# Performance work log

Measured on AMD Instinct MI355X. Metric: run time of the kernel, lower is better.

The kernel has to match this reference:

```python
import jax, jax.numpy as jnp
import numpy as np

N_NODES = 100000
N_EDGES = 1600000
N_QEDGES = 400000
NUM_FEAT = 128
HIDDEN_C = 128
OUT_C = 64
NO_HEADS = 8


def setup_inputs() -> dict:
    key = jax.random.key(0)
    ks = jax.random.split(key, 8)
    x = jax.random.normal(ks[0], (N_NODES, NUM_FEAT), dtype=jnp.float32)
    W1 = jax.random.normal(ks[1], (NUM_FEAT, HIDDEN_C), dtype=jnp.float32) * (1.0 / np.sqrt(NUM_FEAT))
    b1 = jnp.zeros((HIDDEN_C,), dtype=jnp.float32)
    W2 = jax.random.normal(ks[2], (HIDDEN_C, OUT_C * NO_HEADS), dtype=jnp.float32) * (1.0 / np.sqrt(HIDDEN_C))
    b2 = jnp.zeros((OUT_C * NO_HEADS,), dtype=jnp.float32)
    edge_index = jax.random.randint(ks[3], (2, N_EDGES), 0, N_NODES, dtype=jnp.int32)
    q_edge_index = jax.random.randint(ks[4], (2, N_QEDGES), 0, N_NODES, dtype=jnp.int32)
    y = jax.random.randint(ks[5], (N_NODES,), 0, NO_HEADS, dtype=jnp.int32)
    return {"x": x, "W1": W1, "b1": b1, "W2": W2, "b2": b2,
            "edge_index": edge_index, "q_edge_index": q_edge_index, "y": y}


def gcn_conv(x, W, b, src, dst, n):
    """GCNConv: symmetric normalization with implicit self-loops."""
    h = x @ W  # [n, out]
    ones = jnp.ones(src.shape[0], dtype=x.dtype)
    deg = jax.ops.segment_sum(ones, dst, num_segments=n) + 1.0  # self-loop
    dinv = jax.lax.rsqrt(deg)
    norm = dinv[src] * dinv[dst]  # [E]
    agg = jax.ops.segment_sum(h[src] * norm[:, None], dst, num_segments=n)
    agg = agg + h * (dinv * dinv)[:, None]  # self-loop message
    return agg + b


def reference(x, W1, b1, W2, b2, edge_index, q_edge_index, y):
    src, dst = edge_index[0], edge_index[1]
    n = x.shape[0]
    hiddens = jax.nn.relu(gcn_conv(x, W1, b1, src, dst, n))            # [N, H]
    emb = gcn_conv(hiddens, W2, b2, src, dst, n)                        # [N, heads*out]
    emb = emb.reshape(n, NO_HEADS, OUT_C)                               # [N, h, f]
    q_row, q_col = q_edge_index[0], q_edge_index[1]
    preds = jnp.einsum('ehf,ehf->eh', emb[q_row], emb[q_col])           # [Q, h]
    pred_i = jnp.take_along_axis(preds, y[q_row][:, None].astype(jnp.int32), axis=1)[:, 0]
    pred_j = jnp.take_along_axis(preds, y[q_col][:, None].astype(jnp.int32), axis=1)[:, 0]
    pred = (pred_i + pred_j) * 0.5  # multiheads=True branch
    return hiddens, emb, pred_i, pred_j, pred
```

## Files before the change

kernel.cpp:

```cpp
#include <hip/hip_runtime.h>
#include <hip/hip_bf16.h>


#define SCAN_SEG 512

typedef short bf16x8 __attribute__((ext_vector_type(8)));
typedef float f32x4  __attribute__((ext_vector_type(4)));

__device__ __forceinline__ ushort f2bf(float x) {
    return (ushort)(__float_as_uint(x) >> 16);
}
__device__ __forceinline__ float bf2f(ushort h) {
    return __uint_as_float(((unsigned)h) << 16);
}

__global__ void count_kernel(const int* __restrict__ dst, int* __restrict__ cnt, int E) {
    int e = blockIdx.x * blockDim.x + threadIdx.x;
    if (e < E) atomicAdd(&cnt[dst[e]], 1);
}

__global__ __launch_bounds__(256) void blocksum_kernel(const int* __restrict__ cnt,
                                                       int* __restrict__ blocksum, int n) {
    __shared__ int red[4];
    int b = blockIdx.x, t = threadIdx.x;
    int i0 = b * SCAN_SEG + t;
    int s = 0;
    if (i0 < n) s += cnt[i0];
    if (i0 + 256 < n) s += cnt[i0 + 256];
#pragma unroll
    for (int off = 32; off >= 1; off >>= 1) s += __shfl_xor(s, off, 64);
    if ((t & 63) == 0) red[t >> 6] = s;
    __syncthreads();
    if (t == 0) blocksum[b] = red[0] + red[1] + red[2] + red[3];
}

__global__ __launch_bounds__(256) void blockscan_kernel(const int* __restrict__ blocksum,
                                                        int* __restrict__ blockoff, int nb,
                                                        int* __restrict__ row_ptr, int n, int E) {
    __shared__ int s[256];
    int t = threadIdx.x;
    int v = (t < nb) ? blocksum[t] : 0;
    s[t] = v;
    __syncthreads();
    for (int off = 1; off < 256; off <<= 1) {
        int u = (t >= off) ? s[t - off] : 0;
        __syncthreads();
        s[t] += u;
        __syncthreads();
    }
    if (t < nb) blockoff[t] = s[t] - v;
    if (t == 0) row_ptr[n] = E;
}

__global__ __launch_bounds__(256) void csr_ptr_kernel(const int* __restrict__ cnt,
                                                      const int* __restrict__ blockoff,
                                                      int* __restrict__ row_ptr,
                                                      int* __restrict__ cursor,
                                                      float* __restrict__ dinv, int n) {
    __shared__ int s[256];
    int b = blockIdx.x, t = threadIdx.x;
    int i0 = b * SCAN_SEG + 2 * t;
    int c0 = (i0     < n) ? cnt[i0]     : 0;
    int c1 = (i0 + 1 < n) ? cnt[i0 + 1] : 0;
    int pair = c0 + c1;
    s[t] = pair;
    __syncthreads();
    for (int off = 1; off < 256; off <<= 1) {
        int u = (t >= off) ? s[t - off] : 0;
        __syncthreads();
        s[t] += u;
        __syncthreads();
    }
    int excl = s[t] - pair + blockoff[b];
    if (i0 < n) {
        row_ptr[i0] = excl;
        cursor[i0]  = excl;
        dinv[i0]    = rsqrtf((float)(c0 + 1));
    }
    if (i0 + 1 < n) {
        row_ptr[i0 + 1] = excl + c0;
        cursor[i0 + 1]  = excl + c0;
        dinv[i0 + 1]    = rsqrtf((float)(c1 + 1));
    }
}

__global__ void fill_kernel(const int* __restrict__ src, const int* __restrict__ dst,
                            int* __restrict__ cursor, const float* __restrict__ dinv,
                            int* __restrict__ csr_src, float* __restrict__ csr_wt, int E) {
    int e = blockIdx.x * blockDim.x + threadIdx.x;
    if (e < E) {
        int s = src[e], d = dst[e];
        int pos = atomicAdd(&cursor[d], 1);
        csr_src[pos] = s;
        csr_wt[pos]  = dinv[s] * dinv[d];
    }
}

__global__ __launch_bounds__(128) void agg_kernel(const float* __restrict__ feat,
                                                  const int* __restrict__ row_ptr,
                                                  const int* __restrict__ csr_src,
                                                  const float* __restrict__ csr_wt,
                                                  const float* __restrict__ dinv,
                                                  float* __restrict__ out, int n) {
    int node = blockIdx.x;
    int f = threadIdx.x;
    float di = dinv[node];
    float acc = feat[(size_t)node * 128 + f] * di * di;
    int e0 = row_ptr[node], e1 = row_ptr[node + 1];
    int e = e0;
    for (; e + 4 <= e1; e += 4) {
        int s0 = csr_src[e],   s1 = csr_src[e+1], s2 = csr_src[e+2], s3 = csr_src[e+3];
        float w0 = csr_wt[e],  w1 = csr_wt[e+1],  w2 = csr_wt[e+2],  w3 = csr_wt[e+3];
        float v0 = feat[(size_t)s0 * 128 + f];
        float v1 = feat[(size_t)s1 * 128 + f];
        float v2 = feat[(size_t)s2 * 128 + f];
        float v3 = feat[(size_t)s3 * 128 + f];
        acc += v0 * w0 + v1 * w1 + v2 * w2 + v3 * w3;
    }
    for (; e < e1; ++e)
        acc += feat[(size_t)csr_src[e] * 128 + f] * csr_wt[e];
    out[(size_t)node * 128 + f] = acc;
}

__global__ __launch_bounds__(256, 2) void gemm_mfma(const float* __restrict__ X,
                                                    const float* __restrict__ W,
                                                    const float* __restrict__ bias,
                                                    float* __restrict__ C,
                                                    int N, int ldw, int do_relu) {
    __shared__ ushort Xh[128 * 64];
    __shared__ ushort Xl[128 * 64];
    __shared__ ushort Wh[128 * 64];
    __shared__ ushort Wl[128 * 64];

    const int tid  = threadIdx.x;
    const int lane = tid & 63;
    const int wv   = tid >> 6;
    const int wr   = wv >> 1;
    const int wc   = wv & 1;
    const int lr   = lane & 15;
    const int lk   = lane >> 4;
    const int row0   = blockIdx.y * 128;
    const int colOff = blockIdx.x * 128;

    f32x4 acc[4][4];
#pragma unroll
    for (int i = 0; i < 4; ++i)
#pragma unroll
        for (int j = 0; j < 4; ++j)
            acc[i][j] = (f32x4){0.f, 0.f, 0.f, 0.f};

    for (int ph = 0; ph < 2; ++ph) {
        if (ph) __syncthreads();

        {
#pragma unroll
            for (int j = 0; j < 8; ++j) {
                int e   = tid + 256 * j;
                int row = e >> 4;
                int k4  = e & 15;
                int gr  = row0 + row; if (gr >= N) gr = N - 1;
                float4 v = *(const float4*)(X + (size_t)gr * 128 + ph * 64 + k4 * 4);
                ushort4 h, l;
                h.x = f2bf(v.x); h.y = f2bf(v.y); h.z = f2bf(v.z); h.w = f2bf(v.w);
                l.x = f2bf(v.x - bf2f(h.x));
                l.y = f2bf(v.y - bf2f(h.y));
                l.z = f2bf(v.z - bf2f(h.z));
                l.w = f2bf(v.w - bf2f(h.w));
                int byte = row * 128 + ((k4 * 8) ^ ((row & 7) << 4));
                *(ushort4*)((char*)Xh + byte) = h;
                *(ushort4*)((char*)Xl + byte) = l;
            }
        }
        {
            const int c4 = tid & 31;
            const int kg = tid >> 5;
#pragma unroll
            for (int q = 0; q < 2; ++q) {
                int kloc  = kg * 8 + q * 4;
                int kglob = ph * 64 + kloc;
                const float* wp = W + (size_t)kglob * ldw + colOff + c4 * 4;
                float4 v0 = *(const float4*)(wp);
                float4 v1 = *(const float4*)(wp + ldw);
                float4 v2 = *(const float4*)(wp + 2 * (size_t)ldw);
                float4 v3 = *(const float4*)(wp + 3 * (size_t)ldw);
#pragma unroll
                for (int j = 0; j < 4; ++j) {
                    float a0 = (&v0.x)[j], a1 = (&v1.x)[j], a2 = (&v2.x)[j], a3 = (&v3.x)[j];
                    ushort4 h, l;
                    h.x = f2bf(a0); h.y = f2bf(a1); h.z = f2bf(a2); h.w = f2bf(a3);
                    l.x = f2bf(a0 - bf2f(h.x));
                    l.y = f2bf(a1 - bf2f(h.y));
                    l.z = f2bf(a2 - bf2f(h.z));
                    l.w = f2bf(a3 - bf2f(h.w));
                    int col  = c4 * 4 + j;
                    int byte = col * 128 + ((kloc * 2) ^ ((col & 7) << 4));
                    *(ushort4*)((char*)Wh + byte) = h;
                    *(ushort4*)((char*)Wl + byte) = l;
                }
            }
        }
        __syncthreads();

#pragma unroll
        for (int kk = 0; kk < 2; ++kk) {
            const int kb2 = (kk * 32 + lk * 8) * 2;
            bf16x8 ah[4], al[4], bh[4], bl[4];
#pragma unroll
            for (int mi = 0; mi < 4; ++mi) {
                int row  = wr * 64 + mi * 16 + lr;
                int byte = row * 128 + (kb2 ^ ((row & 7) << 4));
                ah[mi] = *(const bf16x8*)((const char*)Xh + byte);
                al[mi] = *(const bf16x8*)((const char*)Xl + byte);
            }
#pragma unroll
            for (int ni = 0; ni < 4; ++ni) {
                int col  = wc * 64 + ni * 16 + lr;
                int byte = col * 128 + (kb2 ^ ((col & 7) << 4));
                bh[ni] = *(const bf16x8*)((const char*)Wh + byte);
                bl[ni] = *(const bf16x8*)((const char*)Wl + byte);
            }
#pragma unroll
            for (int mi = 0; mi < 4; ++mi)
#pragma unroll
                for (int ni = 0; ni < 4; ++ni) {
                    acc[mi][ni] = __builtin_amdgcn_mfma_f32_16x16x32_bf16(
                        ah[mi], bh[ni], acc[mi][ni], 0, 0, 0);
                    acc[mi][ni] = __builtin_amdgcn_mfma_f32_16x16x32_bf16(
                        ah[mi], bl[ni], acc[mi][ni], 0, 0, 0);
                    acc[mi][ni] = __builtin_amdgcn_mfma_f32_16x16x32_bf16(
                        al[mi], bh[ni], acc[mi][ni], 0, 0, 0);
                }
        }
    }

#pragma unroll
    for (int ni = 0; ni < 4; ++ni) {
        int col = colOff + wc * 64 + ni * 16 + lr;
        float bv = bias[col];
#pragma unroll
        for (int mi = 0; mi < 4; ++mi) {
            int rbase = row0 + wr * 64 + mi * 16 + (lane >> 4) * 4;
#pragma unroll
            for (int r = 0; r < 4; ++r) {
                int row = rbase + r;
                if (row < N) {
                    float v = acc[mi][ni][r] + bv;
                    if (do_relu) v = fmaxf(v, 0.f);
                    C[(size_t)row * ldw + col] = v;
                }
            }
        }
    }
}

__global__ __launch_bounds__(256) void query_kernel(const float* __restrict__ emb,
                                                    const int* __restrict__ qrow,
                                                    const int* __restrict__ qcol,
                                                    const int* __restrict__ y,
                                                    float* __restrict__ pred_i,
                                                    float* __restrict__ pred_j,
                                                    float* __restrict__ pred, int Q) {
    int wave = (int)((blockIdx.x * 256 + threadIdx.x) >> 6);
    int lane = threadIdx.x & 63;
    if (wave >= Q) return;
    int r = qrow[wave], c = qcol[wave];
    int yi = y[r], yj = y[c];
    const float* er = emb + (size_t)r * 512;
    const float* ec = emb + (size_t)c * 512;
    float pi = er[yi * 64 + lane] * ec[yi * 64 + lane];
    float pj = er[yj * 64 + lane] * ec[yj * 64 + lane];
#pragma unroll
    for (int off = 32; off >= 1; off >>= 1) {
        pi += __shfl_xor(pi, off, 64);
        pj += __shfl_xor(pj, off, 64);
    }
    if (lane == 0) {
        pred_i[wave] = pi;
        pred_j[wave] = pj;
        pred[wave]   = 0.5f * (pi + pj);
    }
}

extern "C" void kernel_launch(void* const* d_in, const int* in_sizes, int n_in,
                              void* d_out, int out_size, void* d_ws, size_t ws_size,
                              hipStream_t stream) {
    const float* x   = (const float*)d_in[0];
    const float* W1  = (const float*)d_in[1];
    const float* b1  = (const float*)d_in[2];
    const float* W2  = (const float*)d_in[3];
    const float* b2  = (const float*)d_in[4];
    const int* edge  = (const int*)d_in[5];
    const int* qedge = (const int*)d_in[6];
    const int* y     = (const int*)d_in[7];

    const int N = in_sizes[0] / 128;
    const int E = in_sizes[5] / 2;
    const int Q = in_sizes[6] / 2;

    float* out     = (float*)d_out;
    float* hiddens = out;
    float* emb     = out + (size_t)N * 128;
    float* pred_i  = emb + (size_t)N * 512;
    float* pred_j  = pred_i + Q;
    float* pred    = pred_j + Q;

    char* w = (char*)d_ws;
    auto alloc = [&](size_t bytes) { char* p = w; w += (bytes + 255) & ~(size_t)255; return p; };
    int*   cnt      = (int*)alloc((size_t)N * 4);
    int*   row_ptr  = (int*)alloc((size_t)(N + 1) * 4);
    int*   cursor   = (int*)alloc((size_t)N * 4);
    float* dinv     = (float*)alloc((size_t)N * 4);
    int*   csr_src  = (int*)alloc((size_t)E * 4);
    float* csr_wt   = (float*)alloc((size_t)E * 4);
    int*   blocksum = (int*)alloc(256 * 4);
    int*   blockoff = (int*)alloc(256 * 4);
    float* aggbuf   = (float*)alloc((size_t)N * 128 * 4);

    const int* esrc = edge;         const int* edst = edge + E;
    const int* qrow = qedge;        const int* qcol = qedge + Q;

    const int nb = (N + SCAN_SEG - 1) / SCAN_SEG;

    hipMemsetAsync(cnt, 0, (size_t)N * 4, stream);
    count_kernel<<<dim3((E + 255) / 256), dim3(256), 0, stream>>>(edst, cnt, E);
    blocksum_kernel<<<dim3(nb), dim3(256), 0, stream>>>(cnt, blocksum, N);
    blockscan_kernel<<<dim3(1), dim3(256), 0, stream>>>(blocksum, blockoff, nb, row_ptr, N, E);
    csr_ptr_kernel<<<dim3(nb), dim3(256), 0, stream>>>(cnt, blockoff, row_ptr, cursor, dinv, N);
    fill_kernel<<<dim3((E + 255) / 256), dim3(256), 0, stream>>>(esrc, edst, cursor, dinv, csr_src, csr_wt, E);

    const int mblocks = (N + 127) / 128;

    agg_kernel<<<dim3(N), dim3(128), 0, stream>>>(x, row_ptr, csr_src, csr_wt, dinv, aggbuf, N);
    gemm_mfma<<<dim3(1, mblocks), dim3(256), 0, stream>>>(aggbuf, W1, b1, hiddens, N, 128, 1);

    agg_kernel<<<dim3(N), dim3(128), 0, stream>>>(hiddens, row_ptr, csr_src, csr_wt, dinv, aggbuf, N);
    gemm_mfma<<<dim3(4, mblocks), dim3(256), 0, stream>>>(aggbuf, W2, b2, emb, N, 512, 0);

    query_kernel<<<dim3((Q + 3) / 4), dim3(256), 0, stream>>>(emb, qrow, qcol, y, pred_i, pred_j, pred, Q);
}
```

Measured before the change: 962.5 us.

## Vectorize aggregation per wave, pre-split bf16 hi/lo operands, and vectorize query loads

The aggregation kernel now gives each node one wave, using float4 loads with two half-waves working on alternating edges, and writes its output already split into bf16 high and low parts. Weights are pre-split and transposed once by a new kernel. This lets the GEMM copy ready bf16 tiles into LDS instead of converting fp32 on every tile load. The query kernel gathers its four 64-float rows with float4 loads spread across the quarter-waves. Together these aim to reduce gather-load instruction count and redundant conversion work, at the cost of two extra small launches and an extra workspace buffer.

```diff
diff --git a/kernel.cpp b/kernel.cpp
--- a/kernel.cpp
+++ b/kernel.cpp
@@ -96,34 +96,80 @@
     }
 }
 
-__global__ __launch_bounds__(128) void agg_kernel(const float* __restrict__ feat,
+__global__ __launch_bounds__(256) void wsplit_kernel(const float* __restrict__ W,
+                                                     ushort* __restrict__ th,
+                                                     ushort* __restrict__ tl, int ncols) {
+    int idx = blockIdx.x * 256 + threadIdx.x;
+    if (idx >= 128 * ncols) return;
+    int col = idx >> 7;
+    int k   = idx & 127;
+    float v = W[(size_t)k * ncols + col];
+    ushort h = f2bf(v);
+    th[idx] = h;
+    tl[idx] = f2bf(v - bf2f(h));
+}
+
+__global__ __launch_bounds__(256) void agg_kernel(const float* __restrict__ feat,
                                                   const int* __restrict__ row_ptr,
                                                   const int* __restrict__ csr_src,
                                                   const float* __restrict__ csr_wt,
                                                   const float* __restrict__ dinv,
-                                                  float* __restrict__ out, int n) {
-    int node = blockIdx.x;
-    int f = threadIdx.x;
+                                                  ushort* __restrict__ outh,
+                                                  ushort* __restrict__ outl, int n) {
+    const int w    = threadIdx.x >> 6;
+    const int lane = threadIdx.x & 63;
+    const int node = blockIdx.x * 4 + w;
+    if (node >= n) return;
+    const int g = lane >> 5;
+    const int c = lane & 31;
+
     float di = dinv[node];
-    float acc = feat[(size_t)node * 128 + f] * di * di;
+    float4 acc = make_float4(0.f, 0.f, 0.f, 0.f);
+    if (g == 0) {
+        float4 v = ((const float4*)(feat + (size_t)node * 128))[c];
+        float s2 = di * di;
+        acc.x = v.x * s2; acc.y = v.y * s2; acc.z = v.z * s2; acc.w = v.w * s2;
+    }
+
     int e0 = row_ptr[node], e1 = row_ptr[node + 1];
-    int e = e0;
-    for (; e + 4 <= e1; e += 4) {
-        int s0 = csr_src[e],   s1 = csr_src[e+1], s2 = csr_src[e+2], s3 = csr_src[e+3];
-        float w0 = csr_wt[e],  w1 = csr_wt[e+1],  w2 = csr_wt[e+2],  w3 = csr_wt[e+3];
-        float v0 = feat[(size_t)s0 * 128 + f];
-        float v1 = feat[(size_t)s1 * 128 + f];
-        float v2 = feat[(size_t)s2 * 128 + f];
-        float v3 = feat[(size_t)s3 * 128 + f];
-        acc += v0 * w0 + v1 * w1 + v2 * w2 + v3 * w3;
-    }
-    for (; e < e1; ++e)
-        acc += feat[(size_t)csr_src[e] * 128 + f] * csr_wt[e];
-    out[(size_t)node * 128 + f] = acc;
-}
-
-__global__ __launch_bounds__(256, 2) void gemm_mfma(const float* __restrict__ X,
-                                                    const float* __restrict__ W,
+    int e = e0 + g;
+    for (; e + 2 < e1; e += 4) {
+        int   s0 = csr_src[e],  s1 = csr_src[e + 2];
+        float w0 = csr_wt[e],   w1 = csr_wt[e + 2];
+        float4 v0 = ((const float4*)(feat + (size_t)s0 * 128))[c];
+        float4 v1 = ((const float4*)(feat + (size_t)s1 * 128))[c];
+        acc.x += v0.x * w0 + v1.x * w1;
+        acc.y += v0.y * w0 + v1.y * w1;
+        acc.z += v0.z * w0 + v1.z * w1;
+        acc.w += v0.w * w0 + v1.w * w1;
+    }
+    for (; e < e1; e += 2) {
+        int   s0 = csr_src[e];
+        float w0 = csr_wt[e];
+        float4 v0 = ((const float4*)(feat + (size_t)s0 * 128))[c];
+        acc.x += v0.x * w0; acc.y += v0.y * w0; acc.z += v0.z * w0; acc.w += v0.w * w0;
+    }
+
+    acc.x += __shfl_xor(acc.x, 32, 64);
+    acc.y += __shfl_xor(acc.y, 32, 64);
+    acc.z += __shfl_xor(acc.z, 32, 64);
+    acc.w += __shfl_xor(acc.w, 32, 64);
+
+    if (g == 0) {
+        ushort4 h, l;
+        h.x = f2bf(acc.x); l.x = f2bf(acc.x - bf2f(h.x));
+        h.y = f2bf(acc.y); l.y = f2bf(acc.y - bf2f(h.y));
+        h.z = f2bf(acc.z); l.z = f2bf(acc.z - bf2f(h.z));
+        h.w = f2bf(acc.w); l.w = f2bf(acc.w - bf2f(h.w));
+        *(ushort4*)(outh + (size_t)node * 128 + c * 4) = h;
+        *(ushort4*)(outl + (size_t)node * 128 + c * 4) = l;
+    }
+}
+
+__global__ __launch_bounds__(256, 2) void gemm_mfma(const ushort* __restrict__ Xh_g,
+                                                    const ushort* __restrict__ Xl_g,
+                                                    const ushort* __restrict__ Wth_g,
+                                                    const ushort* __restrict__ Wtl_g,
                                                     const float* __restrict__ bias,
                                                     float* __restrict__ C,
                                                     int N, int ldw, int do_relu) {
@@ -152,52 +198,26 @@
     for (int ph = 0; ph < 2; ++ph) {
         if (ph) __syncthreads();
 
-        {
-#pragma unroll
-            for (int j = 0; j < 8; ++j) {
-                int e   = tid + 256 * j;
-                int row = e >> 4;
-                int k4  = e & 15;
-                int gr  = row0 + row; if (gr >= N) gr = N - 1;
-                float4 v = *(const float4*)(X + (size_t)gr * 128 + ph * 64 + k4 * 4);
-                ushort4 h, l;
-                h.x = f2bf(v.x); h.y = f2bf(v.y); h.z = f2bf(v.z); h.w = f2bf(v.w);
-                l.x = f2bf(v.x - bf2f(h.x));
-                l.y = f2bf(v.y - bf2f(h.y));
-                l.z = f2bf(v.z - bf2f(h.z));
-                l.w = f2bf(v.w - bf2f(h.w));
-                int byte = row * 128 + ((k4 * 8) ^ ((row & 7) << 4));
-                *(ushort4*)((char*)Xh + byte) = h;
-                *(ushort4*)((char*)Xl + byte) = l;
-            }
+#pragma unroll
+        for (int q = 0; q < 4; ++q) {
+            int cidx = tid + 256 * q;
+            int row  = cidx >> 3;
+            int kch  = cidx & 7;
+            int gr   = row0 + row; if (gr >= N) gr = N - 1;
+            size_t ge = (size_t)gr * 128 + ph * 64 + kch * 8;
+            int lb = row * 128 + ((kch * 16) ^ ((row & 7) << 4));
+            *(int4*)((char*)Xh + lb) = *(const int4*)(Xh_g + ge);
+            *(int4*)((char*)Xl + lb) = *(const int4*)(Xl_g + ge);
         }
-        {
-            const int c4 = tid & 31;
-            const int kg = tid >> 5;
-#pragma unroll
-            for (int q = 0; q < 2; ++q) {
-                int kloc  = kg * 8 + q * 4;
-                int kglob = ph * 64 + kloc;
-                const float* wp = W + (size_t)kglob * ldw + colOff + c4 * 4;
-                float4 v0 = *(const float4*)(wp);
-                float4 v1 = *(const float4*)(wp + ldw);
-                float4 v2 = *(const float4*)(wp + 2 * (size_t)ldw);
-                float4 v3 = *(const float4*)(wp + 3 * (size_t)ldw);
-#pragma unroll
-                for (int j = 0; j < 4; ++j) {
-                    float a0 = (&v0.x)[j], a1 = (&v1.x)[j], a2 = (&v2.x)[j], a3 = (&v3.x)[j];
-                    ushort4 h, l;
-                    h.x = f2bf(a0); h.y = f2bf(a1); h.z = f2bf(a2); h.w = f2bf(a3);
-                    l.x = f2bf(a0 - bf2f(h.x));
-                    l.y = f2bf(a1 - bf2f(h.y));
-                    l.z = f2bf(a2 - bf2f(h.z));
-                    l.w = f2bf(a3 - bf2f(h.w));
-                    int col  = c4 * 4 + j;
-                    int byte = col * 128 + ((kloc * 2) ^ ((col & 7) << 4));
-                    *(ushort4*)((char*)Wh + byte) = h;
-                    *(ushort4*)((char*)Wl + byte) = l;
-                }
-            }
+#pragma unroll
+        for (int q = 0; q < 4; ++q) {
+            int cidx = tid + 256 * q;
+            int col  = cidx >> 3;
+            int kch  = cidx & 7;
+            size_t ge = (size_t)(colOff + col) * 128 + ph * 64 + kch * 8;
+            int lb = col * 128 + ((kch * 16) ^ ((col & 7) << 4));
+            *(int4*)((char*)Wh + lb) = *(const int4*)(Wth_g + ge);
+            *(int4*)((char*)Wl + lb) = *(const int4*)(Wtl_g + ge);
         }
         __syncthreads();
 
@@ -264,20 +284,26 @@
     int lane = threadIdx.x & 63;
     if (wave >= Q) return;
     int r = qrow[wave], c = qcol[wave];
-    int yi = y[r], yj = y[c];
-    const float* er = emb + (size_t)r * 512;
-    const float* ec = emb + (size_t)c * 512;
-    float pi = er[yi * 64 + lane] * ec[yi * 64 + lane];
-    float pj = er[yj * 64 + lane] * ec[yj * 64 + lane];
-#pragma unroll
-    for (int off = 32; off >= 1; off >>= 1) {
-        pi += __shfl_xor(pi, off, 64);
-        pj += __shfl_xor(pj, off, 64);
-    }
+    int yr = y[r], yc = y[c];
+    int g = lane >> 4;
+    int t = lane & 15;
+    int node = (g & 1) ? c : r;
+    int head = (g >> 1) ? yc : yr;
+    const float4* p = (const float4*)(emb + (size_t)node * 512 + head * 64);
+    float4 v = p[t];
+    float4 o;
+    o.x = __shfl_xor(v.x, 16, 64);
+    o.y = __shfl_xor(v.y, 16, 64);
+    o.z = __shfl_xor(v.z, 16, 64);
+    o.w = __shfl_xor(v.w, 16, 64);
+    float s = v.x * o.x + v.y * o.y + v.z * o.z + v.w * o.w;
+#pragma unroll
+    for (int off = 8; off >= 1; off >>= 1) s += __shfl_xor(s, off, 64);
+    float other = __shfl_xor(s, 32, 64);
     if (lane == 0) {
-        pred_i[wave] = pi;
-        pred_j[wave] = pj;
-        pred[wave]   = 0.5f * (pi + pj);
+        pred_i[wave] = s;
+        pred_j[wave] = other;
+        pred[wave]   = 0.5f * (s + other);
     }
 }
 
@@ -306,15 +332,20 @@
 
     char* w = (char*)d_ws;
     auto alloc = [&](size_t bytes) { char* p = w; w += (bytes + 255) & ~(size_t)255; return p; };
-    int*   cnt      = (int*)alloc((size_t)N * 4);
-    int*   row_ptr  = (int*)alloc((size_t)(N + 1) * 4);
-    int*   cursor   = (int*)alloc((size_t)N * 4);
-    float* dinv     = (float*)alloc((size_t)N * 4);
-    int*   csr_src  = (int*)alloc((size_t)E * 4);
-    float* csr_wt   = (float*)alloc((size_t)E * 4);
-    int*   blocksum = (int*)alloc(256 * 4);
-    int*   blockoff = (int*)alloc(256 * 4);
-    float* aggbuf   = (float*)alloc((size_t)N * 128 * 4);
+    int*    cnt      = (int*)alloc((size_t)N * 4);
+    int*    row_ptr  = (int*)alloc((size_t)(N + 1) * 4);
+    int*    cursor   = (int*)alloc((size_t)N * 4);
+    float*  dinv     = (float*)alloc((size_t)N * 4);
+    int*    csr_src  = (int*)alloc((size_t)E * 4);
+    float*  csr_wt   = (float*)alloc((size_t)E * 4);
+    int*    blocksum = (int*)alloc(256 * 4);
+    int*    blockoff = (int*)alloc(256 * 4);
+    ushort* aggh     = (ushort*)alloc((size_t)N * 128 * 2);
+    ushort* aggl     = (ushort*)alloc((size_t)N * 128 * 2);
+    ushort* w1h      = (ushort*)alloc(128 * 128 * 2);
+    ushort* w1l      = (ushort*)alloc(128 * 128 * 2);
+    ushort* w2h      = (ushort*)alloc(128 * 512 * 2);
+    ushort* w2l      = (ushort*)alloc(128 * 512 * 2);
 
     const int* esrc = edge;         const int* edst = edge + E;
     const int* qrow = qedge;        const int* qcol = qedge + Q;
@@ -328,13 +359,17 @@
     csr_ptr_kernel<<<dim3(nb), dim3(256), 0, stream>>>(cnt, blockoff, row_ptr, cursor, dinv, N);
     fill_kernel<<<dim3((E + 255) / 256), dim3(256), 0, stream>>>(esrc, edst, cursor, dinv, csr_src, csr_wt, E);
 
+    wsplit_kernel<<<dim3((128 * 128 + 255) / 256), dim3(256), 0, stream>>>(W1, w1h, w1l, 128);
+    wsplit_kernel<<<dim3((128 * 512 + 255) / 256), dim3(256), 0, stream>>>(W2, w2h, w2l, 512);
+
     const int mblocks = (N + 127) / 128;
-
-    agg_kernel<<<dim3(N), dim3(128), 0, stream>>>(x, row_ptr, csr_src, csr_wt, dinv, aggbuf, N);
-    gemm_mfma<<<dim3(1, mblocks), dim3(256), 0, stream>>>(aggbuf, W1, b1, hiddens, N, 128, 1);
-
-    agg_kernel<<<dim3(N), dim3(128), 0, stream>>>(hiddens, row_ptr, csr_src, csr_wt, dinv, aggbuf, N);
-    gemm_mfma<<<dim3(4, mblocks), dim3(256), 0, stream>>>(aggbuf, W2, b2, emb, N, 512, 0);
+    const int ablocks = (N + 3) / 4;
+
+    agg_kernel<<<dim3(ablocks), dim3(256), 0, stream>>>(x, row_ptr, csr_src, csr_wt, dinv, aggh, aggl, N);
+    gemm_mfma<<<dim3(1, mblocks), dim3(256), 0, stream>>>(aggh, aggl, w1h, w1l, b1, hiddens, N, 128, 1);
+
+    agg_kernel<<<dim3(ablocks), dim3(256), 0, stream>>>(hiddens, row_ptr, csr_src, csr_wt, dinv, aggh, aggl, N);
+    gemm_mfma<<<dim3(4, mblocks), dim3(256), 0, stream>>>(aggh, aggl, w2h, w2l, b2, emb, N, 512, 0);
 
     query_kernel<<<dim3((Q + 3) / 4), dim3(256), 0, stream>>>(emb, qrow, qcol, y, pred_i, pred_j, pred, Q);
 }
```

After: 945.8 us. Within noise of the previous version (-1.7%).
